# Kernel optimization log

Hardware: AMD Instinct MI355X
Metric: run time of the kernel (lower is better)

## Reference

```python
import jax, jax.numpy as jnp
import numpy as np

N = 16384
E = 524288
D_IN = 256
D_OUT = 256


def setup_inputs() -> dict:
    key = jax.random.key(0)
    k1, k2, k3, k4, k5, k6 = jax.random.split(key, 6)
    x = jax.random.normal(k1, (N, D_IN), dtype=jnp.float32)
    edge_index = jax.random.randint(k2, (2, E), 0, N, dtype=jnp.int64)
    W_update = jax.random.normal(k3, (D_OUT, D_IN), dtype=jnp.float32) / np.sqrt(D_IN)
    b_update = jax.random.normal(k4, (D_OUT,), dtype=jnp.float32) * 0.01
    W_aggregate = jax.random.normal(k5, (D_OUT, D_IN), dtype=jnp.float32) / np.sqrt(D_IN)
    b_aggregate = jax.random.normal(k6, (D_OUT,), dtype=jnp.float32) * 0.01
    return {
        "x": x,
        "edge_index": edge_index,
        "W_update": W_update,
        "b_update": b_update,
        "W_aggregate": W_aggregate,
        "b_aggregate": b_aggregate,
    }


def reference(x, edge_index, W_update, b_update, W_aggregate, b_aggregate):
    n = x.shape[0]
    src, dst = edge_index[0], edge_index[1]
    # Dense symmetric 0/1 adjacency built with SET semantics (duplicate edges
    # contribute 1, not their count) -- faithful to the torch indexing assign.
    adj = jnp.zeros((n, n), dtype=x.dtype)
    adj = adj.at[src, dst].set(1.0)
    adj = adj.at[dst, src].set(1.0)
    messages = adj @ x                                   # [N, D_in]
    aggregated = messages @ W_aggregate.T + b_aggregate  # [N, D_out]
    updated = x @ W_update.T + b_update + aggregated     # [N, D_out]
    return updated
```

## Files before the change

kernel.cpp:

```cpp
#include <hip/hip_runtime.h>
#include <hip/hip_fp16.h>

#define NN 16384
#define DD 256
#define CAP 160
#define NB 128
#define BK 64
#define LDAP 72
#define PLP 2099200

typedef __attribute__((ext_vector_type(8))) __bf16 bf16x8;
typedef __attribute__((ext_vector_type(8))) unsigned short u16x8;
typedef __attribute__((ext_vector_type(4))) float f32x4;

__device__ __forceinline__ unsigned short f2bn(float f) {
    __bf16 h = (__bf16)f;
    return __builtin_bit_cast(unsigned short, h);
}

__global__ __launch_bounds__(512) void k_prep(const int* __restrict__ ei,
                                              unsigned short* __restrict__ H,
                                              const float* __restrict__ x,
                                              const float* __restrict__ Wu,
                                              const float* __restrict__ Wa,
                                              unsigned short* __restrict__ xb,
                                              unsigned short* __restrict__ wb,
                                              __half* __restrict__ xab,
                                              int E, int epb) {
    const int b = blockIdx.x;
    const int t = threadIdx.x;

    if (b >= 128) {
        if (b < 192) {
            const int w = b - 128;
#pragma unroll
            for (int i = 0; i < 32; ++i) {
                const int f4 = w * 16384 + i * 512 + t;
                float4 v = *(const float4*)(x + (size_t)f4 * 4);
                ushort4 o;
                o.x = f2bn(v.x); o.y = f2bn(v.y); o.z = f2bn(v.z); o.w = f2bn(v.w);
                *(ushort4*)(xb + (size_t)f4 * 4) = o;
            }
        } else if (b < 200) {
            const int w = b - 192;
            const float* src = (w < 4) ? Wu : Wa;
            unsigned short* dst = wb + ((w < 4) ? 0 : 65536);
            const int c0 = (w & 3) * 4096;
#pragma unroll
            for (int i = 0; i < 8; ++i) {
                const int f4 = c0 + i * 512 + t;
                float4 v = *(const float4*)(src + (size_t)f4 * 4);
                ushort4 o;
                o.x = f2bn(v.x); o.y = f2bn(v.y); o.z = f2bn(v.z); o.w = f2bn(v.w);
                *(ushort4*)(dst + (size_t)f4 * 4) = o;
            }
        } else {
            uint4 z; z.x = 0u; z.y = 0u; z.z = 0u; z.w = 0u;
            ((uint4*)xab)[(size_t)(t >> 8) * (PLP / 8) + (NN * 128 / 8) + (t & 255)] = z;
        }
        return;
    }

    __shared__ unsigned int h[NN / 2];
    for (int i = t; i < NN / 2; i += 512) h[i] = 0u;
    __syncthreads();

    const int e0 = b * epb;
    const int e1 = min(e0 + epb, E);
    for (int e = e0 + t; e < e1; e += 512) {
        const int s = ei[e];
        const int d = ei[E + e];
        atomicAdd(&h[s >> 1], 1u << ((s & 1) << 4));
        atomicAdd(&h[d >> 1], 1u << ((d & 1) << 4));
    }
    __syncthreads();

    unsigned short* Hb = H + (size_t)b * NN;
    for (int r = t; r < NN; r += 512)
        Hb[r] = (unsigned short)((h[r >> 1] >> ((r & 1) << 4)) & 0xffffu);
}

__global__ __launch_bounds__(512) void k_gemm_scan(const unsigned short* __restrict__ xb,
                                                   const unsigned short* __restrict__ wb,
                                                   const float* __restrict__ bu,
                                                   const float* __restrict__ ba,
                                                   unsigned short* __restrict__ H,
                                                   unsigned int* __restrict__ cnt,
                                                   float* __restrict__ out,
                                                   __half* __restrict__ xab) {
    __shared__ __align__(16) unsigned short As[128 * LDAP];
    __shared__ __align__(16) unsigned short Bs[256 * LDAP];

    const int t = threadIdx.x;

    if (blockIdx.x >= 256) {
        const int r = (blockIdx.x - 256) * 512 + t;
        unsigned int base = 0;
#pragma unroll 8
        for (int bb = 0; bb < NB; ++bb) {
            const size_t a = (size_t)bb * NN + r;
            const unsigned int v = H[a];
            H[a] = (unsigned short)base;
            base += v;
        }
        cnt[r] = base;
        return;
    }

    const int lane = t & 63;
    const int wid = t >> 6;
    const int wr = wid >> 2;
    const int wc = wid & 3;
    const int row0 = (blockIdx.x >> 1) << 7;
    const int colp = blockIdx.x & 1;
    const unsigned short* Wsrc = wb + ((size_t)colp << 16);

    f32x4 acc[4][4] = {};

    for (int k0 = 0; k0 < DD; k0 += BK) {
        uint4 ra_[2], rb_[4];
#pragma unroll
        for (int i = 0; i < 2; ++i) {
            const int f = i * 512 + t;
            const int r = f >> 3, s = f & 7;
            ra_[i] = *(const uint4*)(xb + (size_t)(row0 + r) * DD + k0 + s * 8);
        }
#pragma unroll
        for (int i = 0; i < 4; ++i) {
            const int f = i * 512 + t;
            const int r = f >> 3, s = f & 7;
            rb_[i] = *(const uint4*)(Wsrc + (size_t)r * DD + k0 + s * 8);
        }
        __syncthreads();
#pragma unroll
        for (int i = 0; i < 2; ++i) {
            const int f = i * 512 + t;
            const int r = f >> 3, s = f & 7;
            *(uint4*)(&As[r * LDAP + s * 8]) = ra_[i];
        }
#pragma unroll
        for (int i = 0; i < 4; ++i) {
            const int f = i * 512 + t;
            const int r = f >> 3, s = f & 7;
            *(uint4*)(&Bs[r * LDAP + s * 8]) = rb_[i];
        }
        __syncthreads();
#pragma unroll
        for (int kk = 0; kk < 2; ++kk) {
            bf16x8 av[4], bv[4];
#pragma unroll
            for (int f = 0; f < 4; ++f) {
                uint4 ra = *(const uint4*)(&As[(wr * 64 + f * 16 + (lane & 15)) * LDAP + kk * 32 + (lane >> 4) * 8]);
                av[f] = __builtin_bit_cast(bf16x8, ra);
                uint4 rv = *(const uint4*)(&Bs[(wc * 64 + f * 16 + (lane & 15)) * LDAP + kk * 32 + (lane >> 4) * 8]);
                bv[f] = __builtin_bit_cast(bf16x8, rv);
            }
#pragma unroll
            for (int fm = 0; fm < 4; ++fm)
#pragma unroll
                for (int fn = 0; fn < 4; ++fn)
                    acc[fm][fn] = __builtin_amdgcn_mfma_f32_16x16x32_bf16(
                        av[fm], bv[fn], acc[fm][fn], 0, 0, 0);
        }
    }

    const int gr0 = row0 + wr * 64 + ((lane >> 4) << 2);
    const int gc0 = wc * 64 + (lane & 15);
    if (colp == 0) {
#pragma unroll
        for (int fn = 0; fn < 4; ++fn) {
            const int c = gc0 + fn * 16;
            const float bias = bu[c] + ba[c];
#pragma unroll
            for (int fm = 0; fm < 4; ++fm) {
                const int r = gr0 + fm * 16;
#pragma unroll
                for (int i = 0; i < 4; ++i)
                    out[(size_t)(r + i) * DD + c] = acc[fm][fn][i] + bias;
            }
        }
    } else {
#pragma unroll
        for (int fn = 0; fn < 4; ++fn) {
            const int c = gc0 + fn * 16;
            const size_t pbase = (size_t)(c >> 7) * PLP + (c & 127);
#pragma unroll
            for (int fm = 0; fm < 4; ++fm) {
                const int r = gr0 + fm * 16;
#pragma unroll
                for (int i = 0; i < 4; ++i)
                    xab[pbase + (size_t)(r + i) * 128] = __float2half(acc[fm][fn][i]);
            }
        }
    }
}

__global__ __launch_bounds__(512) void k_fill(const int* __restrict__ ei,
                                              const unsigned short* __restrict__ H,
                                              unsigned short* __restrict__ list,
                                              int E, int epb) {
    __shared__ unsigned int off[NN / 2];
    const int b = blockIdx.x;
    const int t = threadIdx.x;
    for (int i = t; i < NN / 2; i += 512) off[i] = 0u;
    __syncthreads();

    const unsigned short* Hb = H + (size_t)b * NN;
    const int e0 = b * epb;
    const int e1 = min(e0 + epb, E);
    for (int e = e0 + t; e < e1; e += 512) {
        const int s = ei[e];
        const int d = ei[E + e];
        const int sh1 = (s & 1) << 4;
        const unsigned int o1 = atomicAdd(&off[s >> 1], 1u << sh1);
        const int p1 = (int)Hb[s] + (int)((o1 >> sh1) & 0xffffu);
        if (p1 < CAP) list[(size_t)s * CAP + p1] = (unsigned short)d;
        const int sh2 = (d & 1) << 4;
        const unsigned int o2 = atomicAdd(&off[d >> 1], 1u << sh2);
        const int p2 = (int)Hb[d] + (int)((o2 >> sh2) & 0xffffu);
        if (p2 < CAP) list[(size_t)d * CAP + p2] = (unsigned short)s;
    }
}

#define ACC4(S, V) { \
    acc[S][0] = __hadd2(acc[S][0], __builtin_bit_cast(__half2, (V).x)); \
    acc[S][1] = __hadd2(acc[S][1], __builtin_bit_cast(__half2, (V).y)); \
    acc[S][2] = __hadd2(acc[S][2], __builtin_bit_cast(__half2, (V).z)); \
    acc[S][3] = __hadd2(acc[S][3], __builtin_bit_cast(__half2, (V).w)); }

__global__ __launch_bounds__(256) void k_gather(const unsigned int* __restrict__ cnt,
                                                const unsigned short* __restrict__ list,
                                                const __half* __restrict__ plane,
                                                float* __restrict__ out,
                                                int outoff) {
    __shared__ unsigned int bmw[4][512];
    __shared__ unsigned short lst[4][CAP];

    const int t = threadIdx.x;
    const int wid = t >> 6;
    const int lane = t & 63;
    const int row = (blockIdx.x << 2) + wid;

    uint4 z4; z4.x = 0u; z4.y = 0u; z4.z = 0u; z4.w = 0u;
    ((uint4*)&bmw[wid][0])[lane] = z4;
    ((uint4*)&bmw[wid][0])[64 + lane] = z4;

    const int m = min((int)cnt[row], CAP);
    const unsigned short* gl = list + (size_t)row * CAP;
    for (int i = lane; i < m; i += 64) {
        int idx = gl[i];
        const unsigned int bit = 1u << (idx & 31);
        const unsigned int old = atomicOr(&bmw[wid][idx >> 5], bit);
        if (old & bit) idx = NN;
        lst[wid][i] = (unsigned short)idx;
    }

    const int lg = lane >> 4;
    const int li = lane & 15;
    __half2 acc[4][4];
    const __half2 z2 = __float2half2_rn(0.0f);
#pragma unroll
    for (int s = 0; s < 4; ++s) { acc[s][0] = z2; acc[s][1] = z2; acc[s][2] = z2; acc[s][3] = z2; }

    int i = 0;
    for (; i + 32 <= m; i += 32) {
        const u16x8 e = *(const u16x8*)(&lst[wid][i + lg * 8]);
        uint4 v[8];
#pragma unroll
        for (int j = 0; j < 8; ++j)
            v[j] = *(const uint4*)(plane + ((size_t)e[j] << 7) + li * 8);
#pragma unroll
        for (int j = 0; j < 8; ++j) ACC4(j & 3, v[j]);
    }
    for (; i + 4 <= m; i += 4) {
        uint4 v = *(const uint4*)(plane + ((size_t)lst[wid][i + lg] << 7) + li * 8);
        ACC4(0, v);
    }
    if (i < m && lg < m - i) {
        uint4 v = *(const uint4*)(plane + ((size_t)lst[wid][i + lg] << 7) + li * 8);
        ACC4(1, v);
    }

#pragma unroll
    for (int k = 0; k < 4; ++k) {
        acc[0][k] = __hadd2(acc[0][k], __hadd2(acc[1][k], __hadd2(acc[2][k], acc[3][k])));
        int v = __builtin_bit_cast(int, acc[0][k]);
        v = __shfl_xor(v, 16, 64);
        acc[0][k] = __hadd2(acc[0][k], __builtin_bit_cast(__half2, v));
        v = __builtin_bit_cast(int, acc[0][k]);
        v = __shfl_xor(v, 32, 64);
        acc[0][k] = __hadd2(acc[0][k], __builtin_bit_cast(__half2, v));
    }

    if (lg == 0) {
        float4* po = (float4*)(out + (size_t)row * DD + outoff + li * 8);
        float4 o0 = po[0], o1 = po[1];
        float2 f;
        f = __half22float2(acc[0][0]); o0.x += f.x; o0.y += f.y;
        f = __half22float2(acc[0][1]); o0.z += f.x; o0.w += f.y;
        f = __half22float2(acc[0][2]); o1.x += f.x; o1.y += f.y;
        f = __half22float2(acc[0][3]); o1.z += f.x; o1.w += f.y;
        po[0] = o0; po[1] = o1;
    }
}

extern "C" void kernel_launch(void* const* d_in, const int* in_sizes, int n_in,
                              void* d_out, int out_size, void* d_ws, size_t ws_size,
                              hipStream_t stream) {
    const float* x  = (const float*)d_in[0];
    const int*   ei = (const int*)d_in[1];
    const float* Wu = (const float*)d_in[2];
    const float* bu = (const float*)d_in[3];
    const float* Wa = (const float*)d_in[4];
    const float* ba = (const float*)d_in[5];
    float* out = (float*)d_out;

    const int E = in_sizes[1] / 2;
    const int epb = (E + NB - 1) / NB;

    char* ws = (char*)d_ws;
    __half* xab = (__half*)ws;
    unsigned short* wb = (unsigned short*)(ws + 8396800);
    unsigned short* xb = (unsigned short*)(ws + 8658944);
    unsigned short* H = (unsigned short*)(ws + 17047552);
    unsigned int* cnt = (unsigned int*)(ws + 21241856);
    unsigned short* list = (unsigned short*)(ws + 21307392);

    k_prep<<<201, 512, 0, stream>>>(ei, H, x, Wu, Wa, xb, wb, xab, E, epb);
    k_gemm_scan<<<288, 512, 0, stream>>>(xb, wb, bu, ba, H, cnt, out, xab);
    k_fill<<<NB, 512, 0, stream>>>(ei, H, list, E, epb);
    k_gather<<<NN / 4, 256, 0, stream>>>(cnt, list, xab, out, 0);
    k_gather<<<NN / 4, 256, 0, stream>>>(cnt, list, xab + PLP, out, 128);
}
```

Before: 112.8 us.

## Split scan into transposing kernel and co-schedule fill with narrower GEMM tiles

Moves the per-row prefix scan into its own kernel, which transposes the histogram through shared memory so that each row's per-block offsets are contiguous. The edge-list fill then runs as extra blocks inside the GEMM launch, overlapping with the matmul and removing one kernel launch. The GEMM tile is narrowed from 256 to 128 output columns, doubling the block count and halving the shared B tile so the fill blocks' shared-memory buffer fits. The costs are an extra kernel, an extra transposed buffer, and scattered 2-byte loads from H2t in the fill loop.

```diff
diff --git a/kernel.cpp b/kernel.cpp
--- a/kernel.cpp
+++ b/kernel.cpp
@@ -80,55 +80,101 @@
         Hb[r] = (unsigned short)((h[r >> 1] >> ((r & 1) << 4)) & 0xffffu);
 }
 
-__global__ __launch_bounds__(512) void k_gemm_scan(const unsigned short* __restrict__ xb,
+__global__ __launch_bounds__(512) void k_scan(const unsigned short* __restrict__ H,
+                                              unsigned short* __restrict__ H2t,
+                                              unsigned int* __restrict__ cnt) {
+    __shared__ unsigned short tile[128][136];
+    const int t = threadIdx.x;
+    const int r0 = blockIdx.x << 7;
+
+#pragma unroll
+    for (int i = 0; i < 4; ++i) {
+        const int f = i * 512 + t;
+        const int bb = f >> 4, q = f & 15;
+        const uint4 v = *(const uint4*)(H + (size_t)bb * NN + r0 + q * 8);
+        *(uint4*)(&tile[bb][q * 8]) = v;
+    }
+    __syncthreads();
+
+    if (t < 128) {
+        unsigned int base = 0;
+#pragma unroll 8
+        for (int bb = 0; bb < 128; ++bb) {
+            const unsigned int v = tile[bb][t];
+            tile[bb][t] = (unsigned short)base;
+            base += v;
+        }
+        cnt[r0 + t] = base;
+    }
+    __syncthreads();
+
+#pragma unroll
+    for (int i = 0; i < 4; ++i) {
+        const int f = i * 512 + t;
+        const int j = f >> 4, q = f & 15;
+        u16x8 o;
+#pragma unroll
+        for (int k = 0; k < 8; ++k) o[k] = tile[q * 8 + k][j];
+        *(u16x8*)(H2t + (size_t)(r0 + j) * 128 + q * 8) = o;
+    }
+}
+
+__global__ __launch_bounds__(512) void k_gemm_fill(const unsigned short* __restrict__ xb,
                                                    const unsigned short* __restrict__ wb,
                                                    const float* __restrict__ bu,
                                                    const float* __restrict__ ba,
-                                                   unsigned short* __restrict__ H,
-                                                   unsigned int* __restrict__ cnt,
+                                                   const int* __restrict__ ei,
+                                                   const unsigned short* __restrict__ H2t,
+                                                   unsigned short* __restrict__ list,
                                                    float* __restrict__ out,
-                                                   __half* __restrict__ xab) {
-    __shared__ __align__(16) unsigned short As[128 * LDAP];
-    __shared__ __align__(16) unsigned short Bs[256 * LDAP];
-
+                                                   __half* __restrict__ xab,
+                                                   int E, int epb) {
+    __shared__ __align__(16) unsigned short smem[2 * 128 * LDAP];
     const int t = threadIdx.x;
 
-    if (blockIdx.x >= 256) {
-        const int r = (blockIdx.x - 256) * 512 + t;
-        unsigned int base = 0;
-#pragma unroll 8
-        for (int bb = 0; bb < NB; ++bb) {
-            const size_t a = (size_t)bb * NN + r;
-            const unsigned int v = H[a];
-            H[a] = (unsigned short)base;
-            base += v;
-        }
-        cnt[r] = base;
+    if (blockIdx.x >= 512) {
+        unsigned int* off = (unsigned int*)smem;
+        const int b = blockIdx.x - 512;
+        for (int i = t; i < NN / 2; i += 512) off[i] = 0u;
+        __syncthreads();
+        const int e0 = b * epb;
+        const int e1 = min(e0 + epb, E);
+        for (int e = e0 + t; e < e1; e += 512) {
+            const int s = ei[e];
+            const int d = ei[E + e];
+            const int sh1 = (s & 1) << 4;
+            const unsigned int o1 = atomicAdd(&off[s >> 1], 1u << sh1);
+            const int p1 = (int)H2t[(size_t)s * 128 + b] + (int)((o1 >> sh1) & 0xffffu);
+            if (p1 < CAP) list[(size_t)s * CAP + p1] = (unsigned short)d;
+            const int sh2 = (d & 1) << 4;
+            const unsigned int o2 = atomicAdd(&off[d >> 1], 1u << sh2);
+            const int p2 = (int)H2t[(size_t)d * 128 + b] + (int)((o2 >> sh2) & 0xffffu);
+            if (p2 < CAP) list[(size_t)d * CAP + p2] = (unsigned short)s;
+        }
         return;
     }
+
+    unsigned short* As = smem;
+    unsigned short* Bs = smem + 128 * LDAP;
 
     const int lane = t & 63;
     const int wid = t >> 6;
     const int wr = wid >> 2;
     const int wc = wid & 3;
-    const int row0 = (blockIdx.x >> 1) << 7;
-    const int colp = blockIdx.x & 1;
-    const unsigned short* Wsrc = wb + ((size_t)colp << 16);
-
-    f32x4 acc[4][4] = {};
+    const int rowp = blockIdx.x >> 2;
+    const int colq = blockIdx.x & 3;
+    const int row0 = rowp << 7;
+    const unsigned short* Wsrc = wb + ((size_t)colq << 15);
+
+    f32x4 acc[4][2] = {};
 
     for (int k0 = 0; k0 < DD; k0 += BK) {
-        uint4 ra_[2], rb_[4];
+        uint4 ra_[2], rb_[2];
 #pragma unroll
         for (int i = 0; i < 2; ++i) {
             const int f = i * 512 + t;
             const int r = f >> 3, s = f & 7;
             ra_[i] = *(const uint4*)(xb + (size_t)(row0 + r) * DD + k0 + s * 8);
-        }
-#pragma unroll
-        for (int i = 0; i < 4; ++i) {
-            const int f = i * 512 + t;
-            const int r = f >> 3, s = f & 7;
             rb_[i] = *(const uint4*)(Wsrc + (size_t)r * DD + k0 + s * 8);
         }
         __syncthreads();
@@ -137,39 +183,37 @@
             const int f = i * 512 + t;
             const int r = f >> 3, s = f & 7;
             *(uint4*)(&As[r * LDAP + s * 8]) = ra_[i];
-        }
-#pragma unroll
-        for (int i = 0; i < 4; ++i) {
-            const int f = i * 512 + t;
-            const int r = f >> 3, s = f & 7;
             *(uint4*)(&Bs[r * LDAP + s * 8]) = rb_[i];
         }
         __syncthreads();
 #pragma unroll
         for (int kk = 0; kk < 2; ++kk) {
-            bf16x8 av[4], bv[4];
+            bf16x8 av[4], bv[2];
 #pragma unroll
             for (int f = 0; f < 4; ++f) {
                 uint4 ra = *(const uint4*)(&As[(wr * 64 + f * 16 + (lane & 15)) * LDAP + kk * 32 + (lane >> 4) * 8]);
                 av[f] = __builtin_bit_cast(bf16x8, ra);
-                uint4 rv = *(const uint4*)(&Bs[(wc * 64 + f * 16 + (lane & 15)) * LDAP + kk * 32 + (lane >> 4) * 8]);
+            }
+#pragma unroll
+            for (int f = 0; f < 2; ++f) {
+                uint4 rv = *(const uint4*)(&Bs[(wc * 32 + f * 16 + (lane & 15)) * LDAP + kk * 32 + (lane >> 4) * 8]);
                 bv[f] = __builtin_bit_cast(bf16x8, rv);
             }
 #pragma unroll
             for (int fm = 0; fm < 4; ++fm)
 #pragma unroll
-                for (int fn = 0; fn < 4; ++fn)
+                for (int fn = 0; fn < 2; ++fn)
                     acc[fm][fn] = __builtin_amdgcn_mfma_f32_16x16x32_bf16(
                         av[fm], bv[fn], acc[fm][fn], 0, 0, 0);
         }
     }
 
     const int gr0 = row0 + wr * 64 + ((lane >> 4) << 2);
-    const int gc0 = wc * 64 + (lane & 15);
-    if (colp == 0) {
-#pragma unroll
-        for (int fn = 0; fn < 4; ++fn) {
-            const int c = gc0 + fn * 16;
+    const int lc0 = wc * 32 + (lane & 15);
+    if (colq < 2) {
+#pragma unroll
+        for (int fn = 0; fn < 2; ++fn) {
+            const int c = (colq << 7) + lc0 + fn * 16;
             const float bias = bu[c] + ba[c];
 #pragma unroll
             for (int fm = 0; fm < 4; ++fm) {
@@ -180,45 +224,18 @@
             }
         }
     } else {
-#pragma unroll
-        for (int fn = 0; fn < 4; ++fn) {
-            const int c = gc0 + fn * 16;
-            const size_t pbase = (size_t)(c >> 7) * PLP + (c & 127);
+        __half* xp = xab + (size_t)(colq - 2) * PLP;
+#pragma unroll
+        for (int fn = 0; fn < 2; ++fn) {
+            const int c = lc0 + fn * 16;
 #pragma unroll
             for (int fm = 0; fm < 4; ++fm) {
                 const int r = gr0 + fm * 16;
 #pragma unroll
                 for (int i = 0; i < 4; ++i)
-                    xab[pbase + (size_t)(r + i) * 128] = __float2half(acc[fm][fn][i]);
-            }
-        }
-    }
-}
-
-__global__ __launch_bounds__(512) void k_fill(const int* __restrict__ ei,
-                                              const unsigned short* __restrict__ H,
-                                              unsigned short* __restrict__ list,
-                                              int E, int epb) {
-    __shared__ unsigned int off[NN / 2];
-    const int b = blockIdx.x;
-    const int t = threadIdx.x;
-    for (int i = t; i < NN / 2; i += 512) off[i] = 0u;
-    __syncthreads();
-
-    const unsigned short* Hb = H + (size_t)b * NN;
-    const int e0 = b * epb;
-    const int e1 = min(e0 + epb, E);
-    for (int e = e0 + t; e < e1; e += 512) {
-        const int s = ei[e];
-        const int d = ei[E + e];
-        const int sh1 = (s & 1) << 4;
-        const unsigned int o1 = atomicAdd(&off[s >> 1], 1u << sh1);
-        const int p1 = (int)Hb[s] + (int)((o1 >> sh1) & 0xffffu);
-        if (p1 < CAP) list[(size_t)s * CAP + p1] = (unsigned short)d;
-        const int sh2 = (d & 1) << 4;
-        const unsigned int o2 = atomicAdd(&off[d >> 1], 1u << sh2);
-        const int p2 = (int)Hb[d] + (int)((o2 >> sh2) & 0xffffu);
-        if (p2 < CAP) list[(size_t)d * CAP + p2] = (unsigned short)s;
+                    xp[(size_t)(r + i) * 128 + c] = __float2half(acc[fm][fn][i]);
+            }
+        }
     }
 }
 
@@ -325,10 +342,11 @@
     unsigned short* H = (unsigned short*)(ws + 17047552);
     unsigned int* cnt = (unsigned int*)(ws + 21241856);
     unsigned short* list = (unsigned short*)(ws + 21307392);
+    unsigned short* H2t = (unsigned short*)(ws + 26550272);
 
     k_prep<<<201, 512, 0, stream>>>(ei, H, x, Wu, Wa, xb, wb, xab, E, epb);
-    k_gemm_scan<<<288, 512, 0, stream>>>(xb, wb, bu, ba, H, cnt, out, xab);
-    k_fill<<<NB, 512, 0, stream>>>(ei, H, list, E, epb);
+    k_scan<<<NN / 128, 512, 0, stream>>>(H, H2t, cnt);
+    k_gemm_fill<<<640, 512, 0, stream>>>(xb, wb, bu, ba, ei, H2t, list, out, xab, E, epb);
     k_gather<<<NN / 4, 256, 0, stream>>>(cnt, list, xab, out, 0);
     k_gather<<<NN / 4, 256, 0, stream>>>(cnt, list, xab + PLP, out, 128);
 }
```

Measured after the change: 109.6 us. 2.8% less time.
